# Performance work log

Measured on AMD Instinct MI355X. Metric: run time of the kernel, lower is better.

## Reference

```python
import jax, jax.numpy as jnp
import numpy as np


def setup_inputs() -> dict:
    key = jax.random.key(0)
    k1, k2 = jax.random.split(key)
    B, F, E = 16384, 200, 64
    features = jax.random.normal(k1, (B, F), dtype=jnp.float32)
    # per-feature Linear(1, E, bias=False) weights, stacked: [F, E]
    W = jax.random.uniform(k2, (F, E), dtype=jnp.float32, minval=-1e-4, maxval=1e-4)
    return {"features": features, "W": W}


def reference(features, W):
    # emb[b, f, e] = features[b, f] * W[f, e]  (rank-1 'Linear(1,E)' per feature)
    # sum over features then square:  (sum_f f_bf * W_fe)^2 = (features @ W)^2
    sum_emb = jnp.einsum('bf,fe->be', features, W)            # [B, E]
    # sum over features of squares: sum_f (f_bf * W_fe)^2 = (features^2) @ (W^2)
    sq_sum = jnp.einsum('bf,fe->be', features * features, W * W)  # [B, E]
    # FM second-order term, summed over embedding dim, keepdim
    predicts = jnp.sum(sum_emb * sum_emb - sq_sum, axis=1, keepdims=True)  # [B, 1]
    return predicts
```

## Files before the change

### kernel.cpp

```cpp
#include <hip/hip_runtime.h>


constexpr int F  = 200;
constexpr int RB = 32;
constexpr int KP = 232;
constexpr float WSCALE = 8192.0f;
constexpr float OSCALE = 1.0f / (WSCALE * WSCALE);

typedef _Float16 half8 __attribute__((ext_vector_type(8)));
typedef _Float16 half4 __attribute__((ext_vector_type(4)));
typedef float floatx4 __attribute__((ext_vector_type(4)));

__global__ __launch_bounds__(256)
void fm_mfma(const float* __restrict__ X, const float* __restrict__ W,
             float* __restrict__ out)
{
    __shared__ alignas(16) _Float16 xt[RB][KP];
    __shared__ alignas(16) _Float16 wt[64][KP];
    __shared__ alignas(16) float    sf[F];
    __shared__ alignas(16) float    res[RB];

    const int t    = threadIdx.x;
    const int lane = t & 63;

    {
        const floatx4* W4 = (const floatx4*)W;
        for (int j = 0; j < 13; ++j) {
            int i = t + 256 * j;
            if (i < 3200) {
                floatx4 w4 = W4[i];
                int f  = i >> 4;
                int e0 = (i & 15) * 4;
                float ss = w4.x*w4.x + w4.y*w4.y + w4.z*w4.z + w4.w*w4.w;
                ss += __shfl_xor(ss, 1, 64);
                ss += __shfl_xor(ss, 2, 64);
                ss += __shfl_xor(ss, 4, 64);
                ss += __shfl_xor(ss, 8, 64);
                if ((t & 15) == 0) sf[f] = ss;
                wt[e0 + 0][f] = (_Float16)(w4.x * WSCALE);
                wt[e0 + 1][f] = (_Float16)(w4.y * WSCALE);
                wt[e0 + 2][f] = (_Float16)(w4.z * WSCALE);
                wt[e0 + 3][f] = (_Float16)(w4.w * WSCALE);
            }
        }
        half8 z = {};
        *(half8*)&wt[t >> 2][200 + 8 * (t & 3)] = z;
        if (t < 128) *(half8*)&xt[t >> 2][200 + 8 * (t & 3)] = z;
    }
    __syncthreads();

    const int rowBase = (int)blockIdx.x * RB;
    {
        int r = t >> 3, sub = t & 7;
        const floatx4* Xr = (const floatx4*)(X + (size_t)(rowBase + r) * F);
        float q = 0.f;
        for (int j = 0; j < 7; ++j) {
            int f4 = sub + 8 * j;
            if (f4 < 50) {
                floatx4 x4 = Xr[f4];
                floatx4 s4 = *(const floatx4*)&sf[4 * f4];
                q += x4.x*x4.x*s4.x + x4.y*x4.y*s4.y + x4.z*x4.z*s4.z + x4.w*x4.w*s4.w;
                half4 h;
                h[0] = (_Float16)x4.x; h[1] = (_Float16)x4.y;
                h[2] = (_Float16)x4.z; h[3] = (_Float16)x4.w;
                *(half4*)&xt[r][4 * f4] = h;
            }
        }
        q += __shfl_xor(q, 1, 64);
        q += __shfl_xor(q, 2, 64);
        q += __shfl_xor(q, 4, 64);
        if (sub == 0) res[r] = -q;
    }
    __syncthreads();

    {
        const int w  = t >> 6;
        const int mt = (w & 1) * 16;
        const int nb = (w >> 1) * 32;
        const int lm = lane & 15, lq = lane >> 4;

        const half8* ap  = (const half8*)&xt[mt + lm][lq * 8];
        const half8* b0p = (const half8*)&wt[nb + lm][lq * 8];
        const half8* b1p = (const half8*)&wt[nb + 16 + lm][lq * 8];

        floatx4 acc0 = {}, acc1 = {};
        #pragma unroll
        for (int kk = 0; kk < 7; ++kk) {
            half8 a  = ap [kk * 4];
            half8 b0 = b0p[kk * 4];
            half8 b1 = b1p[kk * 4];
            acc0 = __builtin_amdgcn_mfma_f32_16x16x32_f16(a, b0, acc0, 0, 0, 0);
            acc1 = __builtin_amdgcn_mfma_f32_16x16x32_f16(a, b1, acc1, 0, 0, 0);
        }

        float p[4];
        #pragma unroll
        for (int r2 = 0; r2 < 4; ++r2)
            p[r2] = acc0[r2]*acc0[r2] + acc1[r2]*acc1[r2];
        #pragma unroll
        for (int r2 = 0; r2 < 4; ++r2) {
            p[r2] += __shfl_xor(p[r2], 1, 64);
            p[r2] += __shfl_xor(p[r2], 2, 64);
            p[r2] += __shfl_xor(p[r2], 4, 64);
            p[r2] += __shfl_xor(p[r2], 8, 64);
        }
        if (lm == 0) {
            #pragma unroll
            for (int r2 = 0; r2 < 4; ++r2)
                atomicAdd(&res[mt + lq * 4 + r2], p[r2] * OSCALE);
        }
    }
    __syncthreads();

    if (t < RB) out[rowBase + t] = res[t];
}

extern "C" void kernel_launch(void* const* d_in, const int* in_sizes, int n_in,
                              void* d_out, int out_size, void* d_ws, size_t ws_size,
                              hipStream_t stream) {
    const float* X = (const float*)d_in[0];
    const float* W = (const float*)d_in[1];
    float* out = (float*)d_out;

    const int B = in_sizes[0] / F;
    fm_mfma<<<B / RB, 256, 0, stream>>>(X, W, out);
}
```

Baseline: 67.54 us.

## Precompute transposed fp16 weights in a prep kernel and prefetch X early

A single-block prep kernel now transposes and converts W to scaled fp16 once, computes the per-feature sum of squares, and writes both to workspace. The main kernel copies the ready-made tile with vectorized loads instead of redoing the scatter-transpose in every block. It also issues the X row loads into registers before the weight copy so their latency overlaps with it. The cost is an extra kernel launch, a serial dependency on one small block, and more register pressure from holding X in registers.

New measurement: 70.36 us. +4.2%, slower.

```diff
diff --git a/kernel.cpp b/kernel.cpp
--- a/kernel.cpp
+++ b/kernel.cpp
@@ -6,13 +6,60 @@
 constexpr int KP = 232;
 constexpr float WSCALE = 8192.0f;
 constexpr float OSCALE = 1.0f / (WSCALE * WSCALE);
+constexpr int WT_HALF8 = 64 * KP / 8;
+constexpr size_t WS_WT_OFF = 1024;
 
 typedef _Float16 half8 __attribute__((ext_vector_type(8)));
 typedef _Float16 half4 __attribute__((ext_vector_type(4)));
 typedef float floatx4 __attribute__((ext_vector_type(4)));
 
 __global__ __launch_bounds__(256)
-void fm_mfma(const float* __restrict__ X, const float* __restrict__ W,
+void fm_prep(const float* __restrict__ W, void* __restrict__ ws)
+{
+    __shared__ alignas(16) _Float16 wt[64][KP];
+    const int t = threadIdx.x;
+
+    half8 z = {};
+    #pragma unroll
+    for (int j = 0; j < 8; ++j) {
+        int c = t + 256 * j;
+        if (c < WT_HALF8) *(half8*)&wt[0][c * 8] = z;
+    }
+    __syncthreads();
+
+    float* sf_out = (float*)ws;
+    const floatx4* W4 = (const floatx4*)W;
+    for (int j = 0; j < 13; ++j) {
+        int i = t + 256 * j;
+        if (i < 3200) {
+            floatx4 w4 = W4[i];
+            int f  = i >> 4;
+            int e0 = (i & 15) * 4;
+            float ss = w4.x*w4.x + w4.y*w4.y + w4.z*w4.z + w4.w*w4.w;
+            ss += __shfl_xor(ss, 1, 64);
+            ss += __shfl_xor(ss, 2, 64);
+            ss += __shfl_xor(ss, 4, 64);
+            ss += __shfl_xor(ss, 8, 64);
+            if ((t & 15) == 0) sf_out[f] = ss;
+            wt[e0 + 0][f] = (_Float16)(w4.x * WSCALE);
+            wt[e0 + 1][f] = (_Float16)(w4.y * WSCALE);
+            wt[e0 + 2][f] = (_Float16)(w4.z * WSCALE);
+            wt[e0 + 3][f] = (_Float16)(w4.w * WSCALE);
+        }
+    }
+    __syncthreads();
+
+    const half8* src = (const half8*)&wt[0][0];
+    half8* dst = (half8*)((char*)ws + WS_WT_OFF);
+    #pragma unroll
+    for (int j = 0; j < 8; ++j) {
+        int c = t + 256 * j;
+        if (c < WT_HALF8) dst[c] = src[c];
+    }
+}
+
+__global__ __launch_bounds__(256)
+void fm_main(const float* __restrict__ X, const void* __restrict__ ws,
              float* __restrict__ out)
 {
     __shared__ alignas(16) _Float16 xt[RB][KP];
@@ -22,42 +69,37 @@
 
     const int t    = threadIdx.x;
     const int lane = t & 63;
+    const int rowBase = (int)blockIdx.x * RB;
+
+    const int r = t >> 3, sub = t & 7;
+    const floatx4* Xr = (const floatx4*)(X + (size_t)(rowBase + r) * F);
+    floatx4 xv[7];
+    #pragma unroll
+    for (int j = 0; j < 7; ++j) {
+        int f4 = sub + 8 * j;
+        if (f4 < 50) xv[j] = Xr[f4];
+        else { floatx4 zz = {}; xv[j] = zz; }
+    }
 
     {
-        const floatx4* W4 = (const floatx4*)W;
-        for (int j = 0; j < 13; ++j) {
-            int i = t + 256 * j;
-            if (i < 3200) {
-                floatx4 w4 = W4[i];
-                int f  = i >> 4;
-                int e0 = (i & 15) * 4;
-                float ss = w4.x*w4.x + w4.y*w4.y + w4.z*w4.z + w4.w*w4.w;
-                ss += __shfl_xor(ss, 1, 64);
-                ss += __shfl_xor(ss, 2, 64);
-                ss += __shfl_xor(ss, 4, 64);
-                ss += __shfl_xor(ss, 8, 64);
-                if ((t & 15) == 0) sf[f] = ss;
-                wt[e0 + 0][f] = (_Float16)(w4.x * WSCALE);
-                wt[e0 + 1][f] = (_Float16)(w4.y * WSCALE);
-                wt[e0 + 2][f] = (_Float16)(w4.z * WSCALE);
-                wt[e0 + 3][f] = (_Float16)(w4.w * WSCALE);
-            }
-        }
+        const half8* wsrc = (const half8*)((const char*)ws + WS_WT_OFF);
+        half8* wdst = (half8*)&wt[0][0];
+        #pragma unroll
+        for (int j = 0; j < 7; ++j) wdst[t + 256 * j] = wsrc[t + 256 * j];
+        if (t < WT_HALF8 - 1792) wdst[1792 + t] = wsrc[1792 + t];
+        if (t < 50) ((floatx4*)sf)[t] = ((const floatx4*)ws)[t];
         half8 z = {};
-        *(half8*)&wt[t >> 2][200 + 8 * (t & 3)] = z;
         if (t < 128) *(half8*)&xt[t >> 2][200 + 8 * (t & 3)] = z;
     }
     __syncthreads();
 
-    const int rowBase = (int)blockIdx.x * RB;
     {
-        int r = t >> 3, sub = t & 7;
-        const floatx4* Xr = (const floatx4*)(X + (size_t)(rowBase + r) * F);
         float q = 0.f;
+        #pragma unroll
         for (int j = 0; j < 7; ++j) {
             int f4 = sub + 8 * j;
             if (f4 < 50) {
-                floatx4 x4 = Xr[f4];
+                floatx4 x4 = xv[j];
                 floatx4 s4 = *(const floatx4*)&sf[4 * f4];
                 q += x4.x*x4.x*s4.x + x4.y*x4.y*s4.y + x4.z*x4.z*s4.z + x4.w*x4.w*s4.w;
                 half4 h;
@@ -123,5 +165,6 @@
     float* out = (float*)d_out;
 
     const int B = in_sizes[0] / F;
-    fm_mfma<<<B / RB, 256, 0, stream>>>(X, W, out);
+    fm_prep<<<1, 256, 0, stream>>>(W, d_ws);
+    fm_main<<<B / RB, 256, 0, stream>>>(X, d_ws, out);
 }
```

## Load W fragments directly into registers, drop shared W tile, prefetch X

Applied to the files above, without the earlier changes.

Each wave now loads its 16-column slice of W straight from global memory into MFMA B-fragment registers, instead of transposing all of W into shared memory. Each wave then computes both 16-row M tiles against its own E slice. X rows are loaded into registers before the first barrier so their latency overlaps the W loads, and the per-feature W² sums are computed by one thread per feature. This cuts LDS use and the scattered transposed LDS stores, but adds strided uncoalesced global reads of W (4-byte loads, stride 64) and more registers per thread.

Result: no change. 68.35 us (+1.2%).

```diff
diff --git a/kernel.cpp b/kernel.cpp
--- a/kernel.cpp
+++ b/kernel.cpp
@@ -2,6 +2,7 @@
 
 
 constexpr int F  = 200;
+constexpr int E  = 64;
 constexpr int RB = 32;
 constexpr int KP = 232;
 constexpr float WSCALE = 8192.0f;
@@ -12,52 +13,68 @@
 typedef float floatx4 __attribute__((ext_vector_type(4)));
 
 __global__ __launch_bounds__(256)
-void fm_mfma(const float* __restrict__ X, const float* __restrict__ W,
-             float* __restrict__ out)
+void fm_v5(const float* __restrict__ X, const float* __restrict__ W,
+           float* __restrict__ out)
 {
     __shared__ alignas(16) _Float16 xt[RB][KP];
-    __shared__ alignas(16) _Float16 wt[64][KP];
     __shared__ alignas(16) float    sf[F];
     __shared__ alignas(16) float    res[RB];
 
     const int t    = threadIdx.x;
     const int lane = t & 63;
+    const int w    = __builtin_amdgcn_readfirstlane(t >> 6);
+    const int rowBase = (int)blockIdx.x * RB;
 
-    {
-        const floatx4* W4 = (const floatx4*)W;
-        for (int j = 0; j < 13; ++j) {
-            int i = t + 256 * j;
-            if (i < 3200) {
-                floatx4 w4 = W4[i];
-                int f  = i >> 4;
-                int e0 = (i & 15) * 4;
-                float ss = w4.x*w4.x + w4.y*w4.y + w4.z*w4.z + w4.w*w4.w;
-                ss += __shfl_xor(ss, 1, 64);
-                ss += __shfl_xor(ss, 2, 64);
-                ss += __shfl_xor(ss, 4, 64);
-                ss += __shfl_xor(ss, 8, 64);
-                if ((t & 15) == 0) sf[f] = ss;
-                wt[e0 + 0][f] = (_Float16)(w4.x * WSCALE);
-                wt[e0 + 1][f] = (_Float16)(w4.y * WSCALE);
-                wt[e0 + 2][f] = (_Float16)(w4.z * WSCALE);
-                wt[e0 + 3][f] = (_Float16)(w4.w * WSCALE);
-            }
+    const int r = t >> 3, sub = t & 7;
+    const floatx4* Xr = (const floatx4*)(X + (size_t)(rowBase + r) * F);
+    floatx4 xv[7];
+    #pragma unroll
+    for (int j = 0; j < 7; ++j) {
+        int f4 = sub + 8 * j;
+        if (f4 < 50) xv[j] = Xr[f4];
+        else { floatx4 zz = {}; xv[j] = zz; }
+    }
+
+    const int lm = lane & 15, lq = lane >> 4;
+    const int e  = w * 16 + lm;
+    float wraw[7][8];
+    #pragma unroll
+    for (int kk = 0; kk < 7; ++kk) {
+        #pragma unroll
+        for (int j = 0; j < 8; ++j) {
+            int f = kk * 32 + lq * 8 + j;
+            wraw[kk][j] = (f < F) ? W[f * E + e] : 0.f;
         }
-        half8 z = {};
-        *(half8*)&wt[t >> 2][200 + 8 * (t & 3)] = z;
-        if (t < 128) *(half8*)&xt[t >> 2][200 + 8 * (t & 3)] = z;
+    }
+    half8 bfrag[7];
+    #pragma unroll
+    for (int kk = 0; kk < 7; ++kk)
+        #pragma unroll
+        for (int j = 0; j < 8; ++j)
+            bfrag[kk][j] = (_Float16)(wraw[kk][j] * WSCALE);
+
+    if (t < F) {
+        const floatx4* Wr = (const floatx4*)(W + t * E);
+        float s0 = 0.f, s1 = 0.f, s2 = 0.f, s3 = 0.f;
+        #pragma unroll
+        for (int j = 0; j < 16; j += 4) {
+            floatx4 a = Wr[j], b = Wr[j + 1], c = Wr[j + 2], d = Wr[j + 3];
+            s0 += a.x*a.x + a.y*a.y + a.z*a.z + a.w*a.w;
+            s1 += b.x*b.x + b.y*b.y + b.z*b.z + b.w*b.w;
+            s2 += c.x*c.x + c.y*c.y + c.z*c.z + c.w*c.w;
+            s3 += d.x*d.x + d.y*d.y + d.z*d.z + d.w*d.w;
+        }
+        sf[t] = (s0 + s1) + (s2 + s3);
     }
     __syncthreads();
 
-    const int rowBase = (int)blockIdx.x * RB;
     {
-        int r = t >> 3, sub = t & 7;
-        const floatx4* Xr = (const floatx4*)(X + (size_t)(rowBase + r) * F);
         float q = 0.f;
+        #pragma unroll
         for (int j = 0; j < 7; ++j) {
             int f4 = sub + 8 * j;
             if (f4 < 50) {
-                floatx4 x4 = Xr[f4];
+                floatx4 x4 = xv[j];
                 floatx4 s4 = *(const floatx4*)&sf[4 * f4];
                 q += x4.x*x4.x*s4.x + x4.y*x4.y*s4.y + x4.z*x4.z*s4.z + x4.w*x4.w*s4.w;
                 half4 h;
@@ -70,44 +87,44 @@
         q += __shfl_xor(q, 2, 64);
         q += __shfl_xor(q, 4, 64);
         if (sub == 0) res[r] = -q;
+        half8 z = {};
+        if (t < 128) *(half8*)&xt[t >> 2][200 + 8 * (t & 3)] = z;
     }
     __syncthreads();
 
     {
-        const int w  = t >> 6;
-        const int mt = (w & 1) * 16;
-        const int nb = (w >> 1) * 32;
-        const int lm = lane & 15, lq = lane >> 4;
-
-        const half8* ap  = (const half8*)&xt[mt + lm][lq * 8];
-        const half8* b0p = (const half8*)&wt[nb + lm][lq * 8];
-        const half8* b1p = (const half8*)&wt[nb + 16 + lm][lq * 8];
-
+        const half8* a0 = (const half8*)&xt[lm][lq * 8];
+        const half8* a1 = (const half8*)&xt[16 + lm][lq * 8];
         floatx4 acc0 = {}, acc1 = {};
         #pragma unroll
         for (int kk = 0; kk < 7; ++kk) {
-            half8 a  = ap [kk * 4];
-            half8 b0 = b0p[kk * 4];
-            half8 b1 = b1p[kk * 4];
-            acc0 = __builtin_amdgcn_mfma_f32_16x16x32_f16(a, b0, acc0, 0, 0, 0);
-            acc1 = __builtin_amdgcn_mfma_f32_16x16x32_f16(a, b1, acc1, 0, 0, 0);
+            acc0 = __builtin_amdgcn_mfma_f32_16x16x32_f16(a0[kk * 4], bfrag[kk], acc0, 0, 0, 0);
+            acc1 = __builtin_amdgcn_mfma_f32_16x16x32_f16(a1[kk * 4], bfrag[kk], acc1, 0, 0, 0);
         }
 
-        float p[4];
-        #pragma unroll
-        for (int r2 = 0; r2 < 4; ++r2)
-            p[r2] = acc0[r2]*acc0[r2] + acc1[r2]*acc1[r2];
+        float p0[4], p1[4];
         #pragma unroll
         for (int r2 = 0; r2 < 4; ++r2) {
-            p[r2] += __shfl_xor(p[r2], 1, 64);
-            p[r2] += __shfl_xor(p[r2], 2, 64);
-            p[r2] += __shfl_xor(p[r2], 4, 64);
-            p[r2] += __shfl_xor(p[r2], 8, 64);
+            p0[r2] = acc0[r2] * acc0[r2];
+            p1[r2] = acc1[r2] * acc1[r2];
+        }
+        #pragma unroll
+        for (int r2 = 0; r2 < 4; ++r2) {
+            p0[r2] += __shfl_xor(p0[r2], 1, 64);
+            p0[r2] += __shfl_xor(p0[r2], 2, 64);
+            p0[r2] += __shfl_xor(p0[r2], 4, 64);
+            p0[r2] += __shfl_xor(p0[r2], 8, 64);
+            p1[r2] += __shfl_xor(p1[r2], 1, 64);
+            p1[r2] += __shfl_xor(p1[r2], 2, 64);
+            p1[r2] += __shfl_xor(p1[r2], 4, 64);
+            p1[r2] += __shfl_xor(p1[r2], 8, 64);
         }
         if (lm == 0) {
             #pragma unroll
-            for (int r2 = 0; r2 < 4; ++r2)
-                atomicAdd(&res[mt + lq * 4 + r2], p[r2] * OSCALE);
+            for (int r2 = 0; r2 < 4; ++r2) {
+                atomicAdd(&res[lq * 4 + r2],      p0[r2] * OSCALE);
+                atomicAdd(&res[16 + lq * 4 + r2], p1[r2] * OSCALE);
+            }
         }
     }
     __syncthreads();
@@ -123,5 +140,5 @@
     float* out = (float*)d_out;
 
     const int B = in_sizes[0] / F;
-    fm_mfma<<<B / RB, 256, 0, stream>>>(X, W, out);
+    fm_v5<<<B / RB, 256, 0, stream>>>(X, W, out);
 }
```

## Double rows per block, prefetch X into registers, write output directly

Applied to the files above, without the earlier changes.

Each block now covers 64 rows instead of 32, which halves the number of blocks and so halves the redundant per-block W staging and conversion. X row loads are issued into registers before the W staging so their global latency overlaps the W work. Each wave owns a full 16-row by 64-column tile, so no cross-wave reduction is needed and the LDS atomics plus the final barrier go away; results are written to global memory directly. This raises register use (13 float4 per thread) and LDS use, and leaves fewer blocks to spread across CUs.

Result: no change. 67.30 us (-0.4%).

```diff
diff --git a/kernel.cpp b/kernel.cpp
--- a/kernel.cpp
+++ b/kernel.cpp
@@ -2,7 +2,7 @@
 
 
 constexpr int F  = 200;
-constexpr int RB = 32;
+constexpr int RB = 64;
 constexpr int KP = 232;
 constexpr float WSCALE = 8192.0f;
 constexpr float OSCALE = 1.0f / (WSCALE * WSCALE);
@@ -12,16 +12,27 @@
 typedef float floatx4 __attribute__((ext_vector_type(4)));
 
 __global__ __launch_bounds__(256)
-void fm_mfma(const float* __restrict__ X, const float* __restrict__ W,
-             float* __restrict__ out)
+void fm_v6(const float* __restrict__ X, const float* __restrict__ W,
+           float* __restrict__ out)
 {
+    __shared__ alignas(16) _Float16 wt[64][KP];
     __shared__ alignas(16) _Float16 xt[RB][KP];
-    __shared__ alignas(16) _Float16 wt[64][KP];
     __shared__ alignas(16) float    sf[F];
     __shared__ alignas(16) float    res[RB];
 
     const int t    = threadIdx.x;
     const int lane = t & 63;
+    const int w    = __builtin_amdgcn_readfirstlane(t >> 6);
+    const int rowBase = (int)blockIdx.x * RB;
+
+    const int r = t >> 2, sub = t & 3;
+    const floatx4* Xr = (const floatx4*)(X + (size_t)(rowBase + r) * F);
+    floatx4 xv[13];
+    #pragma unroll
+    for (int j = 0; j < 13; ++j) {
+        int f4 = sub + 4 * j;
+        if (f4 < 50) xv[j] = Xr[f4];
+    }
 
     {
         const floatx4* W4 = (const floatx4*)W;
@@ -45,58 +56,63 @@
         }
         half8 z = {};
         *(half8*)&wt[t >> 2][200 + 8 * (t & 3)] = z;
-        if (t < 128) *(half8*)&xt[t >> 2][200 + 8 * (t & 3)] = z;
+        *(half8*)&xt[t >> 2][200 + 8 * (t & 3)] = z;
+    }
+
+    #pragma unroll
+    for (int j = 0; j < 13; ++j) {
+        int f4 = sub + 4 * j;
+        if (f4 < 50) {
+            floatx4 x4 = xv[j];
+            half4 h;
+            h[0] = (_Float16)x4.x; h[1] = (_Float16)x4.y;
+            h[2] = (_Float16)x4.z; h[3] = (_Float16)x4.w;
+            *(half4*)&xt[r][4 * f4] = h;
+        }
     }
     __syncthreads();
 
-    const int rowBase = (int)blockIdx.x * RB;
     {
-        int r = t >> 3, sub = t & 7;
-        const floatx4* Xr = (const floatx4*)(X + (size_t)(rowBase + r) * F);
         float q = 0.f;
-        for (int j = 0; j < 7; ++j) {
-            int f4 = sub + 8 * j;
+        #pragma unroll
+        for (int j = 0; j < 13; ++j) {
+            int f4 = sub + 4 * j;
             if (f4 < 50) {
-                floatx4 x4 = Xr[f4];
+                floatx4 x4 = xv[j];
                 floatx4 s4 = *(const floatx4*)&sf[4 * f4];
                 q += x4.x*x4.x*s4.x + x4.y*x4.y*s4.y + x4.z*x4.z*s4.z + x4.w*x4.w*s4.w;
-                half4 h;
-                h[0] = (_Float16)x4.x; h[1] = (_Float16)x4.y;
-                h[2] = (_Float16)x4.z; h[3] = (_Float16)x4.w;
-                *(half4*)&xt[r][4 * f4] = h;
             }
         }
         q += __shfl_xor(q, 1, 64);
         q += __shfl_xor(q, 2, 64);
-        q += __shfl_xor(q, 4, 64);
         if (sub == 0) res[r] = -q;
+    }
+
+    const int lm = lane & 15, lq = lane >> 4;
+    floatx4 acc0 = {}, acc1 = {}, acc2 = {}, acc3 = {};
+    {
+        const half8* ap = (const half8*)&xt[16 * w + lm][lq * 8];
+        const half8* b0 = (const half8*)&wt[ 0 + lm][lq * 8];
+        const half8* b1 = (const half8*)&wt[16 + lm][lq * 8];
+        const half8* b2 = (const half8*)&wt[32 + lm][lq * 8];
+        const half8* b3 = (const half8*)&wt[48 + lm][lq * 8];
+        #pragma unroll
+        for (int kk = 0; kk < 7; ++kk) {
+            half8 a = ap[kk * 4];
+            acc0 = __builtin_amdgcn_mfma_f32_16x16x32_f16(a, b0[kk * 4], acc0, 0, 0, 0);
+            acc1 = __builtin_amdgcn_mfma_f32_16x16x32_f16(a, b1[kk * 4], acc1, 0, 0, 0);
+            acc2 = __builtin_amdgcn_mfma_f32_16x16x32_f16(a, b2[kk * 4], acc2, 0, 0, 0);
+            acc3 = __builtin_amdgcn_mfma_f32_16x16x32_f16(a, b3[kk * 4], acc3, 0, 0, 0);
+        }
     }
     __syncthreads();
 
     {
-        const int w  = t >> 6;
-        const int mt = (w & 1) * 16;
-        const int nb = (w >> 1) * 32;
-        const int lm = lane & 15, lq = lane >> 4;
-
-        const half8* ap  = (const half8*)&xt[mt + lm][lq * 8];
-        const half8* b0p = (const half8*)&wt[nb + lm][lq * 8];
-        const half8* b1p = (const half8*)&wt[nb + 16 + lm][lq * 8];
-
-        floatx4 acc0 = {}, acc1 = {};
-        #pragma unroll
-        for (int kk = 0; kk < 7; ++kk) {
-            half8 a  = ap [kk * 4];
-            half8 b0 = b0p[kk * 4];
-            half8 b1 = b1p[kk * 4];
-            acc0 = __builtin_amdgcn_mfma_f32_16x16x32_f16(a, b0, acc0, 0, 0, 0);
-            acc1 = __builtin_amdgcn_mfma_f32_16x16x32_f16(a, b1, acc1, 0, 0, 0);
-        }
-
         float p[4];
         #pragma unroll
         for (int r2 = 0; r2 < 4; ++r2)
-            p[r2] = acc0[r2]*acc0[r2] + acc1[r2]*acc1[r2];
+            p[r2] = acc0[r2]*acc0[r2] + acc1[r2]*acc1[r2]
+                  + acc2[r2]*acc2[r2] + acc3[r2]*acc3[r2];
         #pragma unroll
         for (int r2 = 0; r2 < 4; ++r2) {
             p[r2] += __shfl_xor(p[r2], 1, 64);
@@ -106,13 +122,12 @@
         }
         if (lm == 0) {
             #pragma unroll
-            for (int r2 = 0; r2 < 4; ++r2)
-                atomicAdd(&res[mt + lq * 4 + r2], p[r2] * OSCALE);
+            for (int r2 = 0; r2 < 4; ++r2) {
+                int row = 16 * w + lq * 4 + r2;
+                out[rowBase + row] = fmaf(p[r2], OSCALE, res[row]);
+            }
         }
     }
-    __syncthreads();
-
-    if (t < RB) out[rowBase + t] = res[t];
 }
 
 extern "C" void kernel_launch(void* const* d_in, const int* in_sizes, int n_in,
@@ -123,5 +138,5 @@
     float* out = (float*)d_out;
 
     const int B = in_sizes[0] / F;
-    fm_mfma<<<B / RB, 256, 0, stream>>>(X, W, out);
+    fm_v6<<<B / RB, 256, 0, stream>>>(X, W, out);
 }
```
